# Kernel tuning notes

Measured on AMD Instinct MI355X. Metric: run time of the kernel, lower is better.

The kernel has to match this reference:

```python
import jax, jax.numpy as jnp
import numpy as np

HEADS = 16
D_K = 64  # hidden_units // heads


def setup_inputs() -> dict:
    key = jax.random.key(0)
    ks = jax.random.split(key, 9)
    B, S, D, H = 4, 2048, 1024, 1024  # batch, seq, in_shape, hidden_units
    inputs = jax.random.normal(ks[0], (B, S, D), dtype=jnp.float32)
    # xavier_normal for weights, default bias init ~ small uniform (use zeros for simplicity of baseline? keep uniform like torch)
    def xavier(k, fan_in, fan_out):
        std = jnp.sqrt(2.0 / (fan_in + fan_out))
        return jax.random.normal(k, (fan_out, fan_in), dtype=jnp.float32) * std
    Wq = xavier(ks[1], D, H)
    Wk = xavier(ks[2], D, H)
    Wv = xavier(ks[3], D, H)
    Wo = xavier(ks[4], H, H)
    bound = 1.0 / jnp.sqrt(D)
    bq = jax.random.uniform(ks[5], (H,), minval=-bound, maxval=bound, dtype=jnp.float32)
    bk = jax.random.uniform(ks[6], (H,), minval=-bound, maxval=bound, dtype=jnp.float32)
    bv = jax.random.uniform(ks[7], (H,), minval=-bound, maxval=bound, dtype=jnp.float32)
    bo = jax.random.uniform(ks[8], (H,), minval=-1.0 / jnp.sqrt(H), maxval=1.0 / jnp.sqrt(H), dtype=jnp.float32)
    return {"inputs": inputs, "Wq": Wq, "bq": bq, "Wk": Wk, "bk": bk,
            "Wv": Wv, "bv": bv, "Wo": Wo, "bo": bo}


def reference(inputs, Wq, bq, Wk, bk, Wv, bv, Wo, bo):
    B, S, _ = inputs.shape
    # QKV projections -> (B, S, heads, d_k)
    def proj(W, b):
        return (inputs @ W.T + b).reshape(B, S, HEADS, D_K)
    q = proj(Wq, bq)
    k = proj(Wk, bk)
    v = proj(Wv, bv)
    scale = 1.0 / jnp.sqrt(jnp.float32(D_K))
    # scores: (B, heads, S, S)
    scores = jnp.einsum('bqhd,bkhd->bhqk', q, k) * scale
    attn = jax.nn.softmax(scores, axis=-1)
    # (B, heads, S, d_k) -> (B, S, heads*d_k)
    ctx = jnp.einsum('bhqk,bkhd->bqhd', attn, v).reshape(B, S, HEADS * D_K)
    out = ctx @ Wo.T + bo
    return out
```

## Files before the change

kernel.cpp:

```cpp
#include <hip/hip_runtime.h>
#include <stdint.h>


using bf16x8 = __attribute__((ext_vector_type(8))) short;
using f32x4  = __attribute__((ext_vector_type(4))) float;

#define QSCALE 0.18033688f

__device__ __forceinline__ unsigned short f2bf(float f) {
    unsigned u = __builtin_bit_cast(unsigned, f);
    u += 0x7fffu + ((u >> 16) & 1u);
    return (unsigned short)(u >> 16);
}

__device__ __forceinline__ unsigned pack2bf(float f0, float f1) {
    unsigned u0 = __builtin_bit_cast(unsigned, f0) + 0x8000u;
    unsigned u1 = __builtin_bit_cast(unsigned, f1) + 0x8000u;
    return __builtin_amdgcn_perm(u1, u0, 0x07060302);
}

__device__ __forceinline__ void gld16(const void* g, void* l) {
    void* gnc = (void*)g;
    __builtin_amdgcn_global_load_lds((__attribute__((address_space(1))) void*)gnc,
                                     (__attribute__((address_space(3))) void*)l,
                                     16, 0, 0);
}

__device__ __forceinline__ int swz(int R, int g) {
    return R * 64 + ((g ^ (R & 7)) << 3);
}

__global__ void castall(const float* __restrict__ X, const float* __restrict__ Wq,
                        const float* __restrict__ Wk, const float* __restrict__ Wv,
                        const float* __restrict__ Wo, unsigned short* __restrict__ Xb,
                        unsigned short* __restrict__ Wqkvb, unsigned short* __restrict__ Wob) {
    const int bx = blockIdx.x;
    const float* src; unsigned short* dst; int idx;
    if (bx < 8192) { src = X; dst = Xb; idx = bx * 256 + threadIdx.x; }
    else {
        const int r = bx - 8192, w = r >> 10;
        idx = (r & 1023) * 256 + threadIdx.x;
        src = (w == 0) ? Wq : (w == 1) ? Wk : (w == 2) ? Wv : Wo;
        dst = (w == 3) ? Wob : Wqkvb + (size_t)w * 1048576;
    }
    float4 v = ((const float4*)src)[idx];
    ((uint2*)dst)[idx] = make_uint2(pack2bf(v.x, v.y), pack2bf(v.z, v.w));
}

__global__ __launch_bounds__(512, 2) void gemm_qkv(const unsigned short* __restrict__ A,
                                                   const unsigned short* __restrict__ Wqkv,
                                                   const float* __restrict__ bq,
                                                   const float* __restrict__ bk,
                                                   const float* __restrict__ bv,
                                                   unsigned short* __restrict__ Qb,
                                                   unsigned short* __restrict__ Kb,
                                                   unsigned short* __restrict__ Vt) {
    __shared__ alignas(16) unsigned short smem[65536];

    const int tid  = threadIdx.x;
    const int lane = tid & 63;
    const int w    = tid >> 6;
    const int quad = lane >> 4;
    const int l15  = lane & 15;
    const int lr   = lane >> 3;
    const int lcs  = (((lane & 7) ^ lr) << 3);
    const int wm   = w >> 2;
    const int wn   = w & 3;

    int wg = blockIdx.x;
    wg = (wg & 7) * 48 + (wg >> 3);
    const int bxx = wg % 12, byy = wg / 12;
    const int col0 = bxx * 256;
    const int row0 = byy * 256;

    const unsigned short* aS = A    + (size_t)(row0 + w * 16 + lr) * 1024 + lcs;
    const unsigned short* bS = Wqkv + (size_t)(col0 + w * 16 + lr) * 1024 + lcs;
    const int dstW = w * 1024;

#define STG_A(t_, h_, b_)                                                              \
    { const unsigned short* s_ = aS + (size_t)(h_) * 131072 + (t_) * 64;               \
      gld16(s_,            &smem[(b_) * 32768 + (h_) * 8192 + dstW]);                  \
      gld16(s_ + 8 * 1024, &smem[(b_) * 32768 + (h_) * 8192 + dstW + 512]); }
#define STG_B(t_, h_, b_)                                                              \
    { const unsigned short* s_ = bS + (size_t)(h_) * 131072 + (t_) * 64;               \
      gld16(s_,            &smem[(b_) * 32768 + 16384 + (h_) * 8192 + dstW]);          \
      gld16(s_ + 8 * 1024, &smem[(b_) * 32768 + 16384 + (h_) * 8192 + dstW + 512]); }

    f32x4 acc[8][4];
#pragma unroll
    for (int i = 0; i < 8; i++)
#pragma unroll
        for (int j = 0; j < 4; j++) acc[i][j] = f32x4{0.f, 0.f, 0.f, 0.f};

    STG_A(0, 0, 0) STG_A(0, 1, 0) STG_B(0, 0, 0) STG_B(0, 1, 0)
    STG_B(1, 0, 1) STG_B(1, 1, 1)
    asm volatile("s_waitcnt vmcnt(4)" ::: "memory");
    __builtin_amdgcn_s_barrier();

    for (int t = 0; t < 16; ++t) {
        const int b = t & 1;
        unsigned short* bufA = smem + b * 32768;
        unsigned short* bufB = bufA + 16384;
        bf16x8 bfr[4][2];
#pragma unroll
        for (int p = 0; p < 4; ++p) {
            bf16x8 afr[2][2];
            if (p == 0) {
#pragma unroll
                for (int nf = 0; nf < 4; ++nf)
#pragma unroll
                    for (int kx = 0; kx < 2; ++kx)
                        bfr[nf][kx] = *(const bf16x8*)&bufB[swz(wn * 64 + nf * 16 + l15, kx * 4 + quad)];
            }
#pragma unroll
            for (int mi = 0; mi < 2; ++mi)
#pragma unroll
                for (int kx = 0; kx < 2; ++kx)
                    afr[mi][kx] = *(const bf16x8*)&bufA[swz(wm * 128 + (p * 2 + mi) * 16 + l15, kx * 4 + quad)];

            if (p == 0)      { if (t < 15) STG_A(t + 1, 0, b ^ 1) }
            else if (p == 1) { if (t < 15) STG_A(t + 1, 1, b ^ 1) }
            else if (p == 2) { if (t < 14) STG_B(t + 2, 0, b) }
            else {
                if (t < 14) {
                    STG_B(t + 2, 1, b)
                    asm volatile("s_waitcnt vmcnt(4)" ::: "memory");
                } else if (t == 14) {
                    asm volatile("s_waitcnt vmcnt(0)" ::: "memory");
                }
            }
            __builtin_amdgcn_s_barrier();
            __builtin_amdgcn_s_setprio(1);
#pragma unroll
            for (int kx = 0; kx < 2; ++kx)
#pragma unroll
                for (int mi = 0; mi < 2; ++mi)
#pragma unroll
                    for (int nf = 0; nf < 4; ++nf)
                        acc[p * 2 + mi][nf] = __builtin_amdgcn_mfma_f32_16x16x32_bf16(
                            afr[mi][kx], bfr[nf][kx], acc[p * 2 + mi][nf], 0, 0, 0);
            __builtin_amdgcn_s_setprio(0);
            __builtin_amdgcn_s_barrier();
        }
    }
#undef STG_A
#undef STG_B

    const int nb   = col0 >> 10;
    const int colq = col0 & 1023;
    const float* bias = (nb == 0) ? bq : (nb == 1) ? bk : bv;

    if (nb != 2) {
        const float sc = (nb == 0) ? QSCALE : 1.0f;
        unsigned short* C = (nb == 0) ? Qb : Kb;
#pragma unroll
        for (int h = 0; h < 2; ++h) {
            if (wm == h) {
#pragma unroll
                for (int mf = 0; mf < 8; ++mf)
#pragma unroll
                    for (int nf = 0; nf < 4; ++nf) {
                        const int ct  = wn * 64 + nf * 16 + l15;
                        const float bvv = bias[colq + ct];
                        const int rt  = mf * 16 + quad * 4;
#pragma unroll
                        for (int r = 0; r < 4; ++r)
                            smem[(rt + r) * 264 + ct] = f2bf((acc[mf][nf][r] + bvv) * sc);
                    }
            }
            __syncthreads();
            const int rr = tid >> 2, qq = tid & 3;
            unsigned short* gdst = C + (size_t)(row0 + h * 128 + rr) * 1024 + colq + qq * 64;
#pragma unroll
            for (int j = 0; j < 8; ++j)
                *(bf16x8*)(gdst + j * 8) = *(const bf16x8*)&smem[rr * 264 + qq * 64 + j * 8];
            if (h == 0) __syncthreads();
        }
    } else {
        const int bb = row0 >> 11, s0 = row0 & 2047;
#pragma unroll
        for (int h = 0; h < 2; ++h) {
            if (wm == h) {
#pragma unroll
                for (int mf = 0; mf < 8; ++mf)
#pragma unroll
                    for (int nf = 0; nf < 4; ++nf) {
                        const int ct  = wn * 64 + nf * 16 + l15;
                        const float bvv = bias[colq + ct];
                        const int st  = mf * 16 + quad * 4;
                        *(uint2*)&smem[ct * 136 + st] =
                            make_uint2(pack2bf(acc[mf][nf][0] + bvv, acc[mf][nf][1] + bvv),
                                       pack2bf(acc[mf][nf][2] + bvv, acc[mf][nf][3] + bvv));
                    }
            }
            __syncthreads();
            const int c = tid >> 1, hs = tid & 1;
            unsigned short* gdst = Vt + ((size_t)(bb * 1024 + colq + c)) * 2048 + s0 + h * 128 + hs * 64;
#pragma unroll
            for (int j = 0; j < 8; ++j)
                *(bf16x8*)(gdst + j * 8) = *(const bf16x8*)&smem[c * 136 + hs * 64 + j * 8];
            if (h == 0) __syncthreads();
        }
    }
}

__global__ __launch_bounds__(512, 2) void gemm_out(const unsigned short* __restrict__ A,
                                                   const unsigned short* __restrict__ W,
                                                   const float* __restrict__ bias,
                                                   float* __restrict__ C) {
    __shared__ alignas(16) unsigned short smem[49152];

    const int tid  = threadIdx.x;
    const int lane = tid & 63;
    const int w    = tid >> 6;
    const int quad = lane >> 4;
    const int l15  = lane & 15;
    const int lr   = lane >> 3;
    const int lcs  = (((lane & 7) ^ lr) << 3);
    const int wm   = w >> 2;
    const int wn   = w & 3;

    int wg = blockIdx.x;
    wg = (wg & 7) * 32 + (wg >> 3);
    const int col0 = (wg & 3) * 256;
    const int row0 = (wg >> 2) * 128;

    const unsigned short* aS = A + (size_t)(row0 + w * 16 + lr) * 1024 + lcs;
    const unsigned short* bS = W + (size_t)(col0 + w * 16 + lr) * 1024 + lcs;
    const int dstW = w * 1024;

#define STG_AO(t_, b_)                                                                  \
    { const unsigned short* s_ = aS + (t_) * 64;                                        \
      gld16(s_,            &smem[(b_) * 24576 + dstW]);                                 \
      gld16(s_ + 8 * 1024, &smem[(b_) * 24576 + dstW + 512]); }
#define STG_BO(t_, h_, b_)                                                              \
    { const unsigned short* s_ = bS + (size_t)(h_) * 131072 + (t_) * 64;                \
      gld16(s_,            &smem[(b_) * 24576 + 8192 + (h_) * 8192 + dstW]);            \
      gld16(s_ + 8 * 1024, &smem[(b_) * 24576 + 8192 + (h_) * 8192 + dstW + 512]); }

    f32x4 acc[4][4];
#pragma unroll
    for (int i = 0; i < 4; i++)
#pragma unroll
        for (int j = 0; j < 4; j++) acc[i][j] = f32x4{0.f, 0.f, 0.f, 0.f};

    STG_AO(0, 0) STG_BO(0, 0, 0) STG_BO(0, 1, 0)
    STG_BO(1, 0, 1) STG_BO(1, 1, 1)
    asm volatile("s_waitcnt vmcnt(4)" ::: "memory");
    __builtin_amdgcn_s_barrier();

    for (int t = 0; t < 16; ++t) {
        const int b = t & 1;
        unsigned short* bufA = smem + b * 24576;
        unsigned short* bufB = bufA + 8192;
        bf16x8 bfr[4][2];
#pragma unroll
        for (int p = 0; p < 4; ++p) {
            bf16x8 afr[2];
            if (p == 0) {
#pragma unroll
                for (int nf = 0; nf < 4; ++nf)
#pragma unroll
                    for (int kx = 0; kx < 2; ++kx)
                        bfr[nf][kx] = *(const bf16x8*)&bufB[swz(wn * 64 + nf * 16 + l15, kx * 4 + quad)];
            }
#pragma unroll
            for (int kx = 0; kx < 2; ++kx)
                afr[kx] = *(const bf16x8*)&bufA[swz(wm * 64 + p * 16 + l15, kx * 4 + quad)];

            if (p == 0)      { if (t < 15) STG_AO(t + 1, b ^ 1) }
            else if (p == 1) { if (t < 14) STG_BO(t + 2, 0, b) }
            else if (p == 2) { if (t < 14) STG_BO(t + 2, 1, b) }
            else {
                if (t < 14)      { asm volatile("s_waitcnt vmcnt(4)" ::: "memory"); }
                else if (t == 14){ asm volatile("s_waitcnt vmcnt(0)" ::: "memory"); }
            }
            __builtin_amdgcn_s_barrier();
            __builtin_amdgcn_s_setprio(1);
#pragma unroll
            for (int kx = 0; kx < 2; ++kx)
#pragma unroll
                for (int nf = 0; nf < 4; ++nf)
                    acc[p][nf] = __builtin_amdgcn_mfma_f32_16x16x32_bf16(
                        afr[kx], bfr[nf][kx], acc[p][nf], 0, 0, 0);
            __builtin_amdgcn_s_setprio(0);
            __builtin_amdgcn_s_barrier();
        }
    }
#undef STG_AO
#undef STG_BO

#pragma unroll
    for (int mf = 0; mf < 4; ++mf) {
#pragma unroll
        for (int nf = 0; nf < 4; ++nf) {
            const int col   = col0 + wn * 64 + nf * 16 + l15;
            const float bvv = bias[col];
            const int rbase = row0 + wm * 64 + mf * 16 + quad * 4;
#pragma unroll
            for (int r = 0; r < 4; r++)
                C[(size_t)(rbase + r) * 1024 + col] = acc[mf][nf][r] + bvv;
        }
    }
}

__global__ __launch_bounds__(512, 4) void attn(const unsigned short* __restrict__ Q,
                                               const unsigned short* __restrict__ K,
                                               const unsigned short* __restrict__ Vt,
                                               unsigned short* __restrict__ Ctx) {
    __shared__ alignas(16) unsigned short Kl[2][4096];
    __shared__ alignas(16) unsigned short Vl[2][4096];
    __shared__ alignas(16) unsigned short Pl[8][2048];

    const int tid  = threadIdx.x;
    const int lane = tid & 63;
    const int wave = tid >> 6;
    const int quad = lane >> 4;
    const int l15  = lane & 15;
    const int lr   = lane >> 3;
    const int lcs  = (((lane & 7) ^ lr) << 3);

    const int qt = blockIdx.x, h = blockIdx.y, b = blockIdx.z;
    const int q0 = qt * 256;
    const size_t tokbase = (size_t)b * 2048;

    const int lo0 = l15 * 64 + (((quad    ) ^ (l15 & 7)) << 3);
    const int lo1 = l15 * 64 + (((quad + 4) ^ (l15 & 7)) << 3);
    int pwoff[4];
#pragma unroll
    for (int nt = 0; nt < 4; ++nt)
        pwoff[nt] = l15 * 64 + ((((nt << 1) | (quad >> 1)) ^ (l15 & 7)) << 3) + ((quad & 1) << 2);
    unsigned short* pw = &Pl[wave][0];

    bf16x8 qa[2][2];
#pragma unroll
    for (int mt = 0; mt < 2; ++mt)
#pragma unroll
        for (int kx = 0; kx < 2; ++kx)
            qa[mt][kx] = *(const bf16x8*)(Q + (tokbase + q0 + wave * 32 + mt * 16 + l15) * 1024 +
                                          h * 64 + kx * 32 + quad * 8);

    f32x4 O[2][4], Osum[2];
#pragma unroll
    for (int mt = 0; mt < 2; ++mt) {
#pragma unroll
        for (int nt = 0; nt < 4; ++nt) O[mt][nt] = f32x4{0.f, 0.f, 0.f, 0.f};
        Osum[mt] = f32x4{0.f, 0.f, 0.f, 0.f};
    }
    const f32x4 z4 = {0.f, 0.f, 0.f, 0.f};
    const bf16x8 vones = {16256, 16256, 16256, 16256, 16256, 16256, 16256, 16256};

#define AT_STAGE(kt_, buf_)                                                                     \
    {                                                                                           \
        const int rr = wave * 8 + lr;                                                           \
        gld16(K + (tokbase + (kt_) * 64 + rr) * 1024 + h * 64 + lcs, &Kl[buf_][wave * 512]);    \
        gld16(Vt + ((size_t)(b * 1024 + h * 64 + rr)) * 2048 + (kt_) * 64 + lcs,                \
              &Vl[buf_][wave * 512]);                                                           \
    }

    AT_STAGE(0, 0)
    for (int kt = 0; kt < 32; ++kt) {
        const int buf = kt & 1;
        __syncthreads();
        if (kt < 31) AT_STAGE(kt + 1, buf ^ 1)
        const unsigned short* kb_base = &Kl[buf][0];
        const unsigned short* vb_base = &Vl[buf][0];

        f32x4 St[4][2];
        {
            bf16x8 kb[4];
#pragma unroll
            for (int nt = 0; nt < 4; ++nt)
                kb[nt] = *(const bf16x8*)&kb_base[lo0 + nt * 1024];
#pragma unroll
            for (int nt = 0; nt < 4; ++nt)
#pragma unroll
                for (int mt = 0; mt < 2; ++mt)
                    St[nt][mt] = __builtin_amdgcn_mfma_f32_16x16x32_bf16(kb[nt], qa[mt][0], z4, 0, 0, 0);
#pragma unroll
            for (int nt = 0; nt < 4; ++nt)
                kb[nt] = *(const bf16x8*)&kb_base[lo1 + nt * 1024];
#pragma unroll
            for (int nt = 0; nt < 4; ++nt)
#pragma unroll
                for (int mt = 0; mt < 2; ++mt)
                    St[nt][mt] = __builtin_amdgcn_mfma_f32_16x16x32_bf16(kb[nt], qa[mt][1], St[nt][mt], 0, 0, 0);
        }

#pragma unroll
        for (int mt = 0; mt < 2; ++mt) {
#pragma unroll
            for (int nt = 0; nt < 4; ++nt) {
                float p0 = __builtin_amdgcn_exp2f(St[nt][mt][0]);
                float p1 = __builtin_amdgcn_exp2f(St[nt][mt][1]);
                float p2 = __builtin_amdgcn_exp2f(St[nt][mt][2]);
                float p3 = __builtin_amdgcn_exp2f(St[nt][mt][3]);
                *(uint2*)&pw[mt * 1024 + pwoff[nt]] =
                    make_uint2(pack2bf(p0, p1), pack2bf(p2, p3));
            }
        }

#pragma unroll
        for (int kx = 0; kx < 2; ++kx) {
            bf16x8 pa[2], vb[4];
#pragma unroll
            for (int mt = 0; mt < 2; ++mt)
                pa[mt] = *(const bf16x8*)&pw[mt * 1024 + (kx ? lo1 : lo0)];
#pragma unroll
            for (int nt = 0; nt < 4; ++nt)
                vb[nt] = *(const bf16x8*)&vb_base[(kx ? lo1 : lo0) + nt * 1024];
#pragma unroll
            for (int mt = 0; mt < 2; ++mt) {
#pragma unroll
                for (int nt = 0; nt < 4; ++nt)
                    O[mt][nt] = __builtin_amdgcn_mfma_f32_16x16x32_bf16(pa[mt], vb[nt], O[mt][nt], 0, 0, 0);
                Osum[mt] = __builtin_amdgcn_mfma_f32_16x16x32_bf16(pa[mt], vones, Osum[mt], 0, 0, 0);
            }
        }
    }
#undef AT_STAGE

#pragma unroll
    for (int mt = 0; mt < 2; ++mt) {
#pragma unroll
        for (int r = 0; r < 4; ++r) {
            const float inv = 1.0f / Osum[mt][r];
            const int row   = q0 + wave * 32 + mt * 16 + quad * 4 + r;
            const size_t base = (tokbase + row) * 1024 + h * 64;
#pragma unroll
            for (int nt = 0; nt < 4; ++nt)
                Ctx[base + nt * 16 + l15] = f2bf(O[mt][nt][r] * inv);
        }
    }
}

extern "C" void kernel_launch(void* const* d_in, const int* in_sizes, int n_in,
                              void* d_out, int out_size, void* d_ws, size_t ws_size,
                              hipStream_t stream) {
    (void)in_sizes; (void)n_in; (void)out_size; (void)ws_size;
    const float* X  = (const float*)d_in[0];
    const float* Wq = (const float*)d_in[1];
    const float* bq = (const float*)d_in[2];
    const float* Wk = (const float*)d_in[3];
    const float* bk = (const float*)d_in[4];
    const float* Wv = (const float*)d_in[5];
    const float* bv = (const float*)d_in[6];
    const float* Wo = (const float*)d_in[7];
    const float* bo = (const float*)d_in[8];

    char* ws = (char*)d_ws;
    unsigned short* Xb    = (unsigned short*)(ws);
    unsigned short* Qb    = (unsigned short*)(ws + (size_t)16 * 1048576);
    unsigned short* Kb    = (unsigned short*)(ws + (size_t)32 * 1048576);
    unsigned short* Vt    = (unsigned short*)(ws + (size_t)48 * 1048576);
    unsigned short* Wqkvb = (unsigned short*)(ws + (size_t)64 * 1048576);
    unsigned short* Wob   = (unsigned short*)(ws + (size_t)70 * 1048576);
    unsigned short* Ctx   = Xb;

    castall<<<dim3(12288), 256, 0, stream>>>(X, Wq, Wk, Wv, Wo, Xb, Wqkvb, Wob);
    gemm_qkv<<<dim3(384), 512, 0, stream>>>(Xb, Wqkvb, bq, bk, bv, Qb, Kb, Vt);
    attn<<<dim3(8, 16, 4), 512, 0, stream>>>(Qb, Kb, Vt, Ctx);
    gemm_out<<<dim3(256), 512, 0, stream>>>(Ctx, Wob, bo, (float*)d_out);
}
```

Measured before the change: 276.6 us.

## Software-pipeline attention loop so QK of next tile overlaps PV of previous

Restructures the attention inner loop so each iteration computes QK^T for tile kt and PV for tile kt-1, with softmax exp of the current scores deferred after both MFMA blocks. V gets a triple buffer so the previous tile's V stays resident while the next is prefetched. s_setprio raises wave priority around the MFMA blocks to interleave matrix and exp work across waves. This costs extra LDS (one more V buffer) and live St registers across iterations, which may pressure occupancy at 4 blocks per CU.

```diff
diff --git a/kernel.cpp b/kernel.cpp
--- a/kernel.cpp
+++ b/kernel.cpp
@@ -309,7 +309,7 @@
                                                const unsigned short* __restrict__ Vt,
                                                unsigned short* __restrict__ Ctx) {
     __shared__ alignas(16) unsigned short Kl[2][4096];
-    __shared__ alignas(16) unsigned short Vl[2][4096];
+    __shared__ alignas(16) unsigned short Vl[3][4096];
     __shared__ alignas(16) unsigned short Pl[8][2048];
 
     const int tid  = threadIdx.x;
@@ -350,75 +350,84 @@
     const f32x4 z4 = {0.f, 0.f, 0.f, 0.f};
     const bf16x8 vones = {16256, 16256, 16256, 16256, 16256, 16256, 16256, 16256};
 
-#define AT_STAGE(kt_, buf_)                                                                     \
+#define AT_STAGE(kt_, kb_, vbuf_)                                                               \
     {                                                                                           \
         const int rr = wave * 8 + lr;                                                           \
-        gld16(K + (tokbase + (kt_) * 64 + rr) * 1024 + h * 64 + lcs, &Kl[buf_][wave * 512]);    \
+        gld16(K + (tokbase + (kt_) * 64 + rr) * 1024 + h * 64 + lcs, &Kl[kb_][wave * 512]);     \
         gld16(Vt + ((size_t)(b * 1024 + h * 64 + rr)) * 2048 + (kt_) * 64 + lcs,                \
-              &Vl[buf_][wave * 512]);                                                           \
-    }
-
-    AT_STAGE(0, 0)
-    for (int kt = 0; kt < 32; ++kt) {
-        const int buf = kt & 1;
+              &Vl[vbuf_][wave * 512]);                                                          \
+    }
+
+#define QK_BLOCK(kbase_)                                                                        \
+    {                                                                                           \
+        bf16x8 kb[4];                                                                           \
+        _Pragma("unroll") for (int nt = 0; nt < 4; ++nt)                                        \
+            kb[nt] = *(const bf16x8*)&(kbase_)[lo0 + nt * 1024];                                \
+        _Pragma("unroll") for (int nt = 0; nt < 4; ++nt)                                        \
+            _Pragma("unroll") for (int mt = 0; mt < 2; ++mt)                                    \
+                St[nt][mt] = __builtin_amdgcn_mfma_f32_16x16x32_bf16(kb[nt], qa[mt][0], z4, 0, 0, 0); \
+        _Pragma("unroll") for (int nt = 0; nt < 4; ++nt)                                        \
+            kb[nt] = *(const bf16x8*)&(kbase_)[lo1 + nt * 1024];                                \
+        _Pragma("unroll") for (int nt = 0; nt < 4; ++nt)                                        \
+            _Pragma("unroll") for (int mt = 0; mt < 2; ++mt)                                    \
+                St[nt][mt] = __builtin_amdgcn_mfma_f32_16x16x32_bf16(kb[nt], qa[mt][1], St[nt][mt], 0, 0, 0); \
+    }
+
+#define PV_BLOCK(vbase_)                                                                        \
+    _Pragma("unroll") for (int kx = 0; kx < 2; ++kx) {                                          \
+        bf16x8 pa[2], vb[4];                                                                    \
+        _Pragma("unroll") for (int mt = 0; mt < 2; ++mt)                                        \
+            pa[mt] = *(const bf16x8*)&pw[mt * 1024 + (kx ? lo1 : lo0)];                         \
+        _Pragma("unroll") for (int nt = 0; nt < 4; ++nt)                                        \
+            vb[nt] = *(const bf16x8*)&(vbase_)[(kx ? lo1 : lo0) + nt * 1024];                   \
+        _Pragma("unroll") for (int mt = 0; mt < 2; ++mt) {                                      \
+            _Pragma("unroll") for (int nt = 0; nt < 4; ++nt)                                    \
+                O[mt][nt] = __builtin_amdgcn_mfma_f32_16x16x32_bf16(pa[mt], vb[nt], O[mt][nt], 0, 0, 0); \
+            Osum[mt] = __builtin_amdgcn_mfma_f32_16x16x32_bf16(pa[mt], vones, Osum[mt], 0, 0, 0); \
+        }                                                                                       \
+    }
+
+#define SM_BLOCK                                                                                \
+    _Pragma("unroll") for (int mt = 0; mt < 2; ++mt) {                                          \
+        _Pragma("unroll") for (int nt = 0; nt < 4; ++nt) {                                      \
+            float p0 = __builtin_amdgcn_exp2f(St[nt][mt][0]);                                   \
+            float p1 = __builtin_amdgcn_exp2f(St[nt][mt][1]);                                   \
+            float p2 = __builtin_amdgcn_exp2f(St[nt][mt][2]);                                   \
+            float p3 = __builtin_amdgcn_exp2f(St[nt][mt][3]);                                   \
+            *(uint2*)&pw[mt * 1024 + pwoff[nt]] =                                               \
+                make_uint2(pack2bf(p0, p1), pack2bf(p2, p3));                                   \
+        }                                                                                       \
+    }
+
+    f32x4 St[4][2];
+
+    AT_STAGE(0, 0, 0)
+    __syncthreads();
+    AT_STAGE(1, 1, 1)
+    QK_BLOCK(&Kl[0][0])
+    SM_BLOCK
+
+    int vprev = 0;
+    int vnext = 2;
+    for (int kt = 1; kt < 32; ++kt) {
         __syncthreads();
-        if (kt < 31) AT_STAGE(kt + 1, buf ^ 1)
-        const unsigned short* kb_base = &Kl[buf][0];
-        const unsigned short* vb_base = &Vl[buf][0];
-
-        f32x4 St[4][2];
-        {
-            bf16x8 kb[4];
-#pragma unroll
-            for (int nt = 0; nt < 4; ++nt)
-                kb[nt] = *(const bf16x8*)&kb_base[lo0 + nt * 1024];
-#pragma unroll
-            for (int nt = 0; nt < 4; ++nt)
-#pragma unroll
-                for (int mt = 0; mt < 2; ++mt)
-                    St[nt][mt] = __builtin_amdgcn_mfma_f32_16x16x32_bf16(kb[nt], qa[mt][0], z4, 0, 0, 0);
-#pragma unroll
-            for (int nt = 0; nt < 4; ++nt)
-                kb[nt] = *(const bf16x8*)&kb_base[lo1 + nt * 1024];
-#pragma unroll
-            for (int nt = 0; nt < 4; ++nt)
-#pragma unroll
-                for (int mt = 0; mt < 2; ++mt)
-                    St[nt][mt] = __builtin_amdgcn_mfma_f32_16x16x32_bf16(kb[nt], qa[mt][1], St[nt][mt], 0, 0, 0);
-        }
-
-#pragma unroll
-        for (int mt = 0; mt < 2; ++mt) {
-#pragma unroll
-            for (int nt = 0; nt < 4; ++nt) {
-                float p0 = __builtin_amdgcn_exp2f(St[nt][mt][0]);
-                float p1 = __builtin_amdgcn_exp2f(St[nt][mt][1]);
-                float p2 = __builtin_amdgcn_exp2f(St[nt][mt][2]);
-                float p3 = __builtin_amdgcn_exp2f(St[nt][mt][3]);
-                *(uint2*)&pw[mt * 1024 + pwoff[nt]] =
-                    make_uint2(pack2bf(p0, p1), pack2bf(p2, p3));
-            }
-        }
-
-#pragma unroll
-        for (int kx = 0; kx < 2; ++kx) {
-            bf16x8 pa[2], vb[4];
-#pragma unroll
-            for (int mt = 0; mt < 2; ++mt)
-                pa[mt] = *(const bf16x8*)&pw[mt * 1024 + (kx ? lo1 : lo0)];
-#pragma unroll
-            for (int nt = 0; nt < 4; ++nt)
-                vb[nt] = *(const bf16x8*)&vb_base[(kx ? lo1 : lo0) + nt * 1024];
-#pragma unroll
-            for (int mt = 0; mt < 2; ++mt) {
-#pragma unroll
-                for (int nt = 0; nt < 4; ++nt)
-                    O[mt][nt] = __builtin_amdgcn_mfma_f32_16x16x32_bf16(pa[mt], vb[nt], O[mt][nt], 0, 0, 0);
-                Osum[mt] = __builtin_amdgcn_mfma_f32_16x16x32_bf16(pa[mt], vones, Osum[mt], 0, 0, 0);
-            }
-        }
-    }
+        if (kt < 31) AT_STAGE(kt + 1, (kt + 1) & 1, vnext)
+        const unsigned short* kbase = &Kl[kt & 1][0];
+        const unsigned short* vbase = &Vl[vprev][0];
+        __builtin_amdgcn_s_setprio(1);
+        QK_BLOCK(kbase)
+        PV_BLOCK(vbase)
+        __builtin_amdgcn_s_setprio(0);
+        SM_BLOCK
+        vprev = (vprev == 2) ? 0 : vprev + 1;
+        vnext = (vnext == 2) ? 0 : vnext + 1;
+    }
+    PV_BLOCK(&Vl[vprev][0])
+
 #undef AT_STAGE
+#undef QK_BLOCK
+#undef PV_BLOCK
+#undef SM_BLOCK
 
 #pragma unroll
     for (int mt = 0; mt < 2; ++mt) {
```

After: 275.8 us. About the same (-0.3%).
